# Kernel optimization log

Measured on AMD Instinct MI355X. Metric: run time of the kernel, lower is better.

Reference implementation:

```python
import jax, jax.numpy as jnp
import numpy as np
import math
from jax import lax

N = 5          # kernel_size (hard-coded PHT assumes 5x5)
K = N // 2     # 2
EPS = 1e-6
THETA = 0.7

def _pht_kernel_np():
    # H_i = cos(2*pi*2*r^2 + 0*theta) on the 5x5 grid, times calibrated spectral weights, plus eps
    coords = np.arange(N, dtype=np.float32) - K
    gv, gu = np.meshgrid(coords, coords, indexing='ij')  # torch.meshgrid default is 'ij'
    r2 = (gu ** 2 + gv ** 2) / (K * K + EPS)
    H = np.cos(2.0 * math.pi * 2.0 * r2).astype(np.float32)
    target = np.zeros((N, N), np.float32)
    target[K, K] = -4.0
    target[K - 1, K] = 1.0
    target[K + 1, K] = 1.0
    target[K, K - 1] = 1.0
    target[K, K + 1] = 1.0
    sw = np.where(target != 0, target / H, 0.0).astype(np.float32)
    return (H * sw + EPS).astype(np.float32)  # (5,5)

def _rotation_maps_np():
    # Replicates rotate_kernel exactly: float32 cos/sin, int() truncation, later (h,w) overwrite.
    angles = np.linspace(0, 2 * np.pi, 8, endpoint=False)
    SH = np.zeros((8, N, N), np.int32)
    SW = np.zeros((8, N, N), np.int32)
    M = np.zeros((8, N, N), np.float32)
    for ai, a in enumerate(angles):
        c = float(np.cos(np.float32(a)))
        s = float(np.sin(np.float32(a)))
        for h in range(N):
            for w in range(N):
                rh = int(h * c + w * (-s))
                rw = int(h * s + w * c)
                if 0 <= rh < N and 0 <= rw < N:
                    SH[ai, rh, rw] = h
                    SW[ai, rh, rw] = w
                    M[ai, rh, rw] = 1.0
    return SH, SW, M

_PHT = jnp.asarray(_pht_kernel_np())                     # (5,5)
_sh, _sw, _m = _rotation_maps_np()
_SH = jnp.asarray(_sh)
_SW = jnp.asarray(_sw)
_MASK = jnp.asarray(_m)

def setup_inputs() -> dict:
    key = jax.random.key(0)
    k1, k2 = jax.random.split(key)
    x = jax.random.normal(k1, (32, 64, 128, 128), dtype=jnp.float32)
    weight = jax.random.normal(k2, (64, 64, 5, 5), dtype=jnp.float32) * 0.05
    alpha = jnp.ones((1,), dtype=jnp.float32)
    return {"x": x, "weight": weight, "alpha": alpha}

def reference(x, weight, alpha):
    # Branch 1: PHT-modulated weight, averaged over 8 SO(2) rotations.
    # pht_kernel is (C_in,1,5,5) with identical values per channel -> broadcast (5,5).
    w_eff = weight * alpha[0] * _PHT[None, None]          # (Co,Ci,5,5)
    # rotated[o,i,a,rh,rw] = w_eff[o,i,SH[a,rh,rw],SW[a,rh,rw]] * MASK
    rotated = w_eff[:, :, _SH, _SW] * _MASK               # (Co,Ci,8,5,5)
    # conv is linear in weight: mean of 8 convs == conv with mean kernel
    mean_k = rotated.mean(axis=2)                         # (Co,Ci,5,5)
    out = lax.conv_general_dilated(
        x, mean_k, window_strides=(1, 1), padding=[(2, 2), (2, 2)],
        dimension_numbers=("NCHW", "OIHW", "NCHW"))
    # Branch 2: 1x1 kernel_diff; rotation of a 1x1 kernel is identity, mean of 8 == single conv.
    kd = weight.sum(axis=(2, 3))                          # (Co,Ci)
    out_diff = jnp.einsum("oi,bihw->bohw", kd, x)
    return out - THETA * out_diff
```

## Files before the change

kernel.cpp:

```cpp
#include <hip/hip_runtime.h>
#include <stdint.h>

typedef __attribute__((ext_vector_type(8))) __bf16 bf16x8;
typedef __attribute__((ext_vector_type(16))) float f32x16;
typedef __attribute__((ext_vector_type(4))) unsigned int u32x4;
typedef __attribute__((ext_vector_type(2))) float f32x2;
typedef unsigned int u32;
typedef unsigned short u16;

#define THETA 0.7f

__host__ __device__ constexpr float pht_val(int q) {
  return (q == 12) ? (-4.0f + 1e-6f)
       : (q == 7 || q == 11 || q == 13 || q == 17) ? (1.0f + 1e-6f)
       : 1e-6f;
}

__device__ __forceinline__ u16 f2bf(float v) {
  u32 u = __builtin_bit_cast(u32, v);
  return (u16)((u + 0x7fffu + ((u >> 16) & 1u)) >> 16);
}

__global__ __launch_bounds__(256) void k_prep(const float* __restrict__ wgt,
                                              const float* __restrict__ alpha,
                                              u16* __restrict__ apack) {
  int t = blockIdx.x * 256 + threadIdx.x;
  int o = t >> 6, ci = t & 63;
  const float* wp = wgt + ((size_t)(o * 64 + ci)) * 25;
  float wv[25], sumw = 0.f;
#pragma unroll
  for (int p = 0; p < 25; ++p) { wv[p] = wp[p]; sumw += wv[p]; }
  float keff[25];
#pragma unroll
  for (int p = 0; p < 25; ++p) keff[p] = pht_val(p) * wv[p];
  constexpr int TP[33] = {0,1,2,3,4,6,7,9,12,13,  0,1,2,3,4,  0, 0, 0,
                          0,5,10,15,20,  0,5,6,10,11,12,15,17,20,21};
  constexpr int TQ[33] = {5,6,12,17,23,10,16,22,20,21,  0,5,10,15,20,  5, 0, 5,
                          0,6,7,8,9,  5,6,2,12,8,4,17,9,23,14};
#pragma unroll
  for (int e = 0; e < 33; ++e) keff[TP[e]] += pht_val(TQ[e]) * wv[TQ[e]];

  float al = alpha[0];
  int kc = ci >> 4, oh = o >> 5;
  int lane = ((ci >> 3) & 1) * 32 + (o & 31);
#pragma unroll
  for (int p = 0; p < 25; ++p) {
    float v = al * (keff[p] * 0.125f);
    if (p == 12) v -= THETA * sumw;
    size_t idx = ((((size_t)p * 4 + kc) * 2 + oh) * 64 + lane) * 8 + (ci & 7);
    apack[idx] = f2bf(v);
  }
}

#define ROWB 9216

#define MM(A, B, C) __builtin_amdgcn_mfma_f32_32x32x16_bf16((A), __builtin_bit_cast(bf16x8, (B)), (C), 0, 0, 0)

#define LDBR(S, DX, KC) do {                                                \
    const char* pb_ = pcol + (DX) * 128;                                    \
    int gx_ = ((((KC) * 2 + lhi) ^ ((l31 + (DX)) & 7)) << 4);               \
    br##S##0 = *(const u32x4*)(pb_ + 0 * ROWB + gx_);                       \
    br##S##1 = *(const u32x4*)(pb_ + 1 * ROWB + gx_);                       \
    br##S##2 = *(const u32x4*)(pb_ + 2 * ROWB + gx_);                       \
    br##S##3 = *(const u32x4*)(pb_ + 3 * ROWB + gx_);                       \
    br##S##4 = *(const u32x4*)(pb_ + 4 * ROWB + gx_);                       \
    br##S##5 = *(const u32x4*)(pb_ + 5 * ROWB + gx_);                       \
    br##S##6 = *(const u32x4*)(pb_ + 6 * ROWB + gx_);                       \
    br##S##7 = *(const u32x4*)(pb_ + 7 * ROWB + gx_);                       \
  } while (0)

#define LDAF(S, DX, KC) do {                                                \
    af##S##0 = apb[(size_t)((0 * 5 + (DX)) * 512 + (KC) * 128)];            \
    af##S##1 = apb[(size_t)((1 * 5 + (DX)) * 512 + (KC) * 128)];            \
    af##S##2 = apb[(size_t)((2 * 5 + (DX)) * 512 + (KC) * 128)];            \
    af##S##3 = apb[(size_t)((3 * 5 + (DX)) * 512 + (KC) * 128)];            \
    af##S##4 = apb[(size_t)((4 * 5 + (DX)) * 512 + (KC) * 128)];            \
  } while (0)

#define BURST(S) do {                                                       \
    bf16x8 A_;                                                              \
    A_ = __builtin_bit_cast(bf16x8, af##S##0);                              \
    a0 = MM(A_, br##S##0, a0); a1 = MM(A_, br##S##1, a1);                   \
    a2 = MM(A_, br##S##2, a2); a3 = MM(A_, br##S##3, a3);                   \
    A_ = __builtin_bit_cast(bf16x8, af##S##1);                              \
    a0 = MM(A_, br##S##1, a0); a1 = MM(A_, br##S##2, a1);                   \
    a2 = MM(A_, br##S##3, a2); a3 = MM(A_, br##S##4, a3);                   \
    A_ = __builtin_bit_cast(bf16x8, af##S##2);                              \
    a0 = MM(A_, br##S##2, a0); a1 = MM(A_, br##S##3, a1);                   \
    a2 = MM(A_, br##S##4, a2); a3 = MM(A_, br##S##5, a3);                   \
    A_ = __builtin_bit_cast(bf16x8, af##S##3);                              \
    a0 = MM(A_, br##S##3, a0); a1 = MM(A_, br##S##4, a1);                   \
    a2 = MM(A_, br##S##5, a2); a3 = MM(A_, br##S##6, a3);                   \
    A_ = __builtin_bit_cast(bf16x8, af##S##4);                              \
    a0 = MM(A_, br##S##4, a0); a1 = MM(A_, br##S##5, a1);                   \
    a2 = MM(A_, br##S##6, a2); a3 = MM(A_, br##S##7, a3);                   \
  } while (0)

#define SGB __builtin_amdgcn_sched_group_barrier
#define SCHED_FULL() do {                                                   \
    SGB(0x020, 5, 0);                           \
    SGB(0x100, 2, 0); SGB(0x008, 5, 0);                                     \
    SGB(0x100, 2, 0); SGB(0x008, 5, 0);                                     \
    SGB(0x100, 2, 0); SGB(0x008, 5, 0);                                     \
    SGB(0x100, 2, 0); SGB(0x008, 5, 0);                                     \
  } while (0)

#define ITER(CUR, NXT, DXN, KCN) do {                                       \
    LDBR(NXT, DXN, KCN); LDAF(NXT, DXN, KCN); BURST(CUR); SCHED_FULL();     \
  } while (0)

#define TWR(RB, C, I2, W)                                                   \
  *(u32*)((RB) + (C) * 128 + ((((I2) >> 2) ^ ((C) & 7)) << 4)               \
          + (((I2) & 3) << 2)) = (W)

__global__ __launch_bounds__(256, 2) void k_conv(const float* __restrict__ x,
                                                 const u32x4* __restrict__ apv,
                                                 float* __restrict__ out) {
  __shared__ char tile[8 * ROWB];
  int bid = blockIdx.x;
  int lg = (bid & 7) * 256 + (bid >> 3);
  int ph = lg & 1, yt = (lg >> 1) & 31, n = lg >> 6;
  int y0 = yt * 4, px0 = ph * 64;
  int tid = threadIdx.x;
  int l = tid & 63;

  {
    const float* xn = x + (size_t)n * 64 * 16384;
    int p = tid & 31;
    int i2g = tid >> 5;
    bool hthr = (tid < 128) && !(tid & 2);
    int hi2 = tid >> 2, hp = tid & 1;
    int hpx = hp ? px0 + 64 : px0 - 2;
    int hc = hp ? 66 : 0;
    bool hvalid = (unsigned)hpx < 128u;
#pragma unroll
    for (int rr = 0; rr < 8; ++rr) {
      int sy = y0 + rr - 2;
      bool rowok = (unsigned)sy < 128u;
      char* rowbase = tile + rr * ROWB;
      const float* xr = xn + (size_t)sy * 128;
#pragma unroll
      for (int m = 0; m < 4; ++m) {
        int i2 = i2g * 4 + m;
        f32x2 va = {0.f, 0.f}, vb = {0.f, 0.f};
        if (rowok) {
          const float* pa = xr + (size_t)(2 * i2) * 16384 + px0 + 2 * p;
          va = *(const f32x2*)pa;
          vb = *(const f32x2*)(pa + 16384);
        }
        u32 w0 = (u32)f2bf(va.x) | ((u32)f2bf(vb.x) << 16);
        u32 w1 = (u32)f2bf(va.y) | ((u32)f2bf(vb.y) << 16);
        int c0 = 2 * p + 2;
        TWR(rowbase, c0, i2, w0);
        TWR(rowbase, c0 + 1, i2, w1);
      }
      if (hthr) {
        f32x2 va = {0.f, 0.f}, vb = {0.f, 0.f};
        if (rowok && hvalid) {
          const float* pa = xr + (size_t)(2 * hi2) * 16384 + hpx;
          va = *(const f32x2*)pa;
          vb = *(const f32x2*)(pa + 16384);
        }
        u32 w0 = (u32)f2bf(va.x) | ((u32)f2bf(vb.x) << 16);
        u32 w1 = (u32)f2bf(va.y) | ((u32)f2bf(vb.y) << 16);
        TWR(rowbase, hc, hi2, w0);
        TWR(rowbase, hc + 1, hi2, w1);
      }
    }
  }

  int wv = tid >> 6;
  int oh = wv >> 1, q32 = wv & 1;
  int l31 = l & 31, lhi = l >> 5;
  const u32x4* apb = apv + (size_t)(oh * 64 + l);
  const char* pcol = tile + (q32 * 32 + l31) * 128;

  u32x4 brA0, brA1, brA2, brA3, brA4, brA5, brA6, brA7;
  u32x4 brB0, brB1, brB2, brB3, brB4, brB5, brB6, brB7;
  u32x4 afA0, afA1, afA2, afA3, afA4;
  u32x4 afB0, afB1, afB2, afB3, afB4;

  LDAF(A, 0, 0);
  __syncthreads();
  LDBR(A, 0, 0);

  f32x16 a0 = 0, a1 = 0, a2 = 0, a3 = 0;

  ITER(A, B, 0, 1);
  ITER(B, A, 0, 2);
  ITER(A, B, 0, 3);
  ITER(B, A, 1, 0);
  ITER(A, B, 1, 1);
  ITER(B, A, 1, 2);
  ITER(A, B, 1, 3);
  ITER(B, A, 2, 0);
  ITER(A, B, 2, 1);
  ITER(B, A, 2, 2);
  ITER(A, B, 2, 3);
  ITER(B, A, 3, 0);
  ITER(A, B, 3, 1);
  ITER(B, A, 3, 2);
  ITER(A, B, 3, 3);
  ITER(B, A, 4, 0);
  ITER(A, B, 4, 1);
  ITER(B, A, 4, 2);
  ITER(A, B, 4, 3);
  BURST(B);

  float* ob = out + ((size_t)(n * 64 + oh * 32) * 128 + y0) * 128
              + px0 + q32 * 32 + l31;
#pragma unroll
  for (int rg = 0; rg < 16; ++rg) {
    int orow = (rg & 3) + 8 * (rg >> 2) + 4 * lhi;
    float* obr = ob + (size_t)orow * 16384;
    obr[0]   = a0[rg];
    obr[128] = a1[rg];
    obr[256] = a2[rg];
    obr[384] = a3[rg];
  }
}

extern "C" void kernel_launch(void* const* d_in, const int* in_sizes, int n_in,
                              void* d_out, int out_size, void* d_ws, size_t ws_size,
                              hipStream_t stream) {
  const float* x     = (const float*)d_in[0];
  const float* wgt   = (const float*)d_in[1];
  const float* alpha = (const float*)d_in[2];
  float* out = (float*)d_out;

  u16* apack = (u16*)d_ws;

  k_prep<<<16,   256, 0, stream>>>(wgt, alpha, apack);
  k_conv<<<2048, 256, 0, stream>>>(x, (const u32x4*)apack, out);
}
```

Before: 126.7 us.

## Halve conv tile width to 32 pixels with 128-thread blocks and wider staging

Each block now covers 32 output pixels instead of 64 and runs 2 waves instead of 4, doubling the grid to 4096 blocks and halving the LDS tile. Input staging is rewritten so each thread loads 8 channels at a pixel pair and writes one 16-byte vector per column, with halo columns handled by the first 16 threads. The aim is more resident blocks and better latency hiding from the smaller LDS footprint, plus fewer, wider LDS stores. The cost is a larger halo fraction, which means more redundant global reads of x per output pixel.

New measurement: 131.4 us. +3.7%, slower.

```diff
diff --git a/kernel.cpp b/kernel.cpp
--- a/kernel.cpp
+++ b/kernel.cpp
@@ -52,7 +52,7 @@
   }
 }
 
-#define ROWB 9216
+#define ROWB 4608
 
 #define MM(A, B, C) __builtin_amdgcn_mfma_f32_32x32x16_bf16((A), __builtin_bit_cast(bf16x8, (B)), (C), 0, 0, 0)
 
@@ -109,71 +109,66 @@
     LDBR(NXT, DXN, KCN); LDAF(NXT, DXN, KCN); BURST(CUR); SCHED_FULL();     \
   } while (0)
 
-#define TWR(RB, C, I2, W)                                                   \
-  *(u32*)((RB) + (C) * 128 + ((((I2) >> 2) ^ ((C) & 7)) << 4)               \
-          + (((I2) & 3) << 2)) = (W)
-
-__global__ __launch_bounds__(256, 2) void k_conv(const float* __restrict__ x,
+#define STAGE_SLOT(CP, GG) do {                                             \
+    int pxb_ = px0 + 2 * (CP) - 2;                                          \
+    bool ok_ = rowok && ((unsigned)pxb_ < 128u);                            \
+    const float* ps_ = xr + (size_t)(8 * (GG)) * 16384 + pxb_;              \
+    f32x2 v0 = {0.f, 0.f}, v1 = {0.f, 0.f}, v2 = {0.f, 0.f}, v3 = {0.f, 0.f}; \
+    f32x2 v4 = {0.f, 0.f}, v5 = {0.f, 0.f}, v6 = {0.f, 0.f}, v7 = {0.f, 0.f}; \
+    if (ok_) {                                                              \
+      v0 = *(const f32x2*)(ps_);                                            \
+      v1 = *(const f32x2*)(ps_ + 16384);                                    \
+      v2 = *(const f32x2*)(ps_ + 2 * 16384);                                \
+      v3 = *(const f32x2*)(ps_ + 3 * 16384);                                \
+      v4 = *(const f32x2*)(ps_ + 4 * 16384);                                \
+      v5 = *(const f32x2*)(ps_ + 5 * 16384);                                \
+      v6 = *(const f32x2*)(ps_ + 6 * 16384);                                \
+      v7 = *(const f32x2*)(ps_ + 7 * 16384);                                \
+    }                                                                       \
+    u32x4 wx_, wy_;                                                         \
+    wx_[0] = (u32)f2bf(v0.x) | ((u32)f2bf(v1.x) << 16);                     \
+    wx_[1] = (u32)f2bf(v2.x) | ((u32)f2bf(v3.x) << 16);                     \
+    wx_[2] = (u32)f2bf(v4.x) | ((u32)f2bf(v5.x) << 16);                     \
+    wx_[3] = (u32)f2bf(v6.x) | ((u32)f2bf(v7.x) << 16);                     \
+    wy_[0] = (u32)f2bf(v0.y) | ((u32)f2bf(v1.y) << 16);                     \
+    wy_[1] = (u32)f2bf(v2.y) | ((u32)f2bf(v3.y) << 16);                     \
+    wy_[2] = (u32)f2bf(v4.y) | ((u32)f2bf(v5.y) << 16);                     \
+    wy_[3] = (u32)f2bf(v6.y) | ((u32)f2bf(v7.y) << 16);                     \
+    int c0_ = 2 * (CP);                                                     \
+    *(u32x4*)(rowbase + c0_ * 128 + (((GG) ^ (c0_ & 7)) << 4)) = wx_;       \
+    *(u32x4*)(rowbase + (c0_ + 1) * 128 + (((GG) ^ ((c0_ + 1) & 7)) << 4)) = wy_; \
+  } while (0)
+
+__global__ __launch_bounds__(128, 2) void k_conv(const float* __restrict__ x,
                                                  const u32x4* __restrict__ apv,
                                                  float* __restrict__ out) {
   __shared__ char tile[8 * ROWB];
   int bid = blockIdx.x;
-  int lg = (bid & 7) * 256 + (bid >> 3);
-  int ph = lg & 1, yt = (lg >> 1) & 31, n = lg >> 6;
-  int y0 = yt * 4, px0 = ph * 64;
+  int lg = (bid & 7) * 512 + (bid >> 3);
+  int pxq = lg & 3, yt = (lg >> 2) & 31, n = lg >> 7;
+  int y0 = yt * 4, px0 = pxq * 32;
   int tid = threadIdx.x;
   int l = tid & 63;
 
   {
-    const float* xn = x + (size_t)n * 64 * 16384;
-    int p = tid & 31;
-    int i2g = tid >> 5;
-    bool hthr = (tid < 128) && !(tid & 2);
-    int hi2 = tid >> 2, hp = tid & 1;
-    int hpx = hp ? px0 + 64 : px0 - 2;
-    int hc = hp ? 66 : 0;
-    bool hvalid = (unsigned)hpx < 128u;
+    const float* xn = x + (size_t)n * (64 * 16384);
+    int sp = tid & 15, sg = tid >> 4;
+    int hp = 16 + (tid >> 3), hg = tid & 7;
 #pragma unroll
     for (int rr = 0; rr < 8; ++rr) {
       int sy = y0 + rr - 2;
       bool rowok = (unsigned)sy < 128u;
       char* rowbase = tile + rr * ROWB;
       const float* xr = xn + (size_t)sy * 128;
-#pragma unroll
-      for (int m = 0; m < 4; ++m) {
-        int i2 = i2g * 4 + m;
-        f32x2 va = {0.f, 0.f}, vb = {0.f, 0.f};
-        if (rowok) {
-          const float* pa = xr + (size_t)(2 * i2) * 16384 + px0 + 2 * p;
-          va = *(const f32x2*)pa;
-          vb = *(const f32x2*)(pa + 16384);
-        }
-        u32 w0 = (u32)f2bf(va.x) | ((u32)f2bf(vb.x) << 16);
-        u32 w1 = (u32)f2bf(va.y) | ((u32)f2bf(vb.y) << 16);
-        int c0 = 2 * p + 2;
-        TWR(rowbase, c0, i2, w0);
-        TWR(rowbase, c0 + 1, i2, w1);
-      }
-      if (hthr) {
-        f32x2 va = {0.f, 0.f}, vb = {0.f, 0.f};
-        if (rowok && hvalid) {
-          const float* pa = xr + (size_t)(2 * hi2) * 16384 + hpx;
-          va = *(const f32x2*)pa;
-          vb = *(const f32x2*)(pa + 16384);
-        }
-        u32 w0 = (u32)f2bf(va.x) | ((u32)f2bf(vb.x) << 16);
-        u32 w1 = (u32)f2bf(va.y) | ((u32)f2bf(vb.y) << 16);
-        TWR(rowbase, hc, hi2, w0);
-        TWR(rowbase, hc + 1, hi2, w1);
-      }
+      STAGE_SLOT(sp, sg);
+      if (tid < 16) STAGE_SLOT(hp, hg);
     }
   }
 
-  int wv = tid >> 6;
-  int oh = wv >> 1, q32 = wv & 1;
+  int oh = tid >> 6;
   int l31 = l & 31, lhi = l >> 5;
   const u32x4* apb = apv + (size_t)(oh * 64 + l);
-  const char* pcol = tile + (q32 * 32 + l31) * 128;
+  const char* pcol = tile + l31 * 128;
 
   u32x4 brA0, brA1, brA2, brA3, brA4, brA5, brA6, brA7;
   u32x4 brB0, brB1, brB2, brB3, brB4, brB5, brB6, brB7;
@@ -208,7 +203,7 @@
   BURST(B);
 
   float* ob = out + ((size_t)(n * 64 + oh * 32) * 128 + y0) * 128
-              + px0 + q32 * 32 + l31;
+              + px0 + l31;
 #pragma unroll
   for (int rg = 0; rg < 16; ++rg) {
     int orow = (rg & 3) + 8 * (rg >> 2) + 4 * lhi;
@@ -231,5 +226,5 @@
   u16* apack = (u16*)d_ws;
 
   k_prep<<<16,   256, 0, stream>>>(wgt, alpha, apack);
-  k_conv<<<2048, 256, 0, stream>>>(x, (const u32x4*)apack, out);
-}
+  k_conv<<<4096, 128, 0, stream>>>(x, (const u32x4*)apack, out);
+}
```

## Pipeline input tile staging per channel chunk with MFMA compute

Applied to the files above, without the earlier changes.

Restructures the conv kernel so the input tile is loaded and converted to bf16 in four channel chunks, with the global loads and LDS writes of the next chunk interleaved between the MFMA iterations of the current chunk. The loop order changes to run channel chunk outermost and kernel column innermost, with a barrier after each phase. Loads become wider float4 accesses per thread and use the hardware packed bf16 convert instruction, and the tile column layout is shifted by two for alignment. The aim is to hide the global-load and convert prologue behind compute, at the cost of more barriers, more register pressure and a more complex schedule.

New measurement: 116.2 us. -8.3%, faster.

```diff
diff --git a/kernel.cpp b/kernel.cpp
--- a/kernel.cpp
+++ b/kernel.cpp
@@ -4,6 +4,7 @@
 typedef __attribute__((ext_vector_type(8))) __bf16 bf16x8;
 typedef __attribute__((ext_vector_type(16))) float f32x16;
 typedef __attribute__((ext_vector_type(4))) unsigned int u32x4;
+typedef __attribute__((ext_vector_type(4))) float f32x4;
 typedef __attribute__((ext_vector_type(2))) float f32x2;
 typedef unsigned int u32;
 typedef unsigned short u16;
@@ -56,9 +57,13 @@
 
 #define MM(A, B, C) __builtin_amdgcn_mfma_f32_32x32x16_bf16((A), __builtin_bit_cast(bf16x8, (B)), (C), 0, 0, 0)
 
+#define PK2(A_, B_) ({ u32 r_;                                              \
+    asm("v_cvt_pk_bf16_f32 %0, %1, %2" : "=v"(r_) : "v"(A_), "v"(B_));      \
+    r_; })
+
 #define LDBR(S, DX, KC) do {                                                \
     const char* pb_ = pcol + (DX) * 128;                                    \
-    int gx_ = ((((KC) * 2 + lhi) ^ ((l31 + (DX)) & 7)) << 4);               \
+    int gx_ = ((((KC) * 2 + lhi) ^ ((l31 + (DX) + 2) & 7)) << 4);           \
     br##S##0 = *(const u32x4*)(pb_ + 0 * ROWB + gx_);                       \
     br##S##1 = *(const u32x4*)(pb_ + 1 * ROWB + gx_);                       \
     br##S##2 = *(const u32x4*)(pb_ + 2 * ROWB + gx_);                       \
@@ -98,7 +103,7 @@
 
 #define SGB __builtin_amdgcn_sched_group_barrier
 #define SCHED_FULL() do {                                                   \
-    SGB(0x020, 5, 0);                           \
+    SGB(0x020, 5, 0);                                                       \
     SGB(0x100, 2, 0); SGB(0x008, 5, 0);                                     \
     SGB(0x100, 2, 0); SGB(0x008, 5, 0);                                     \
     SGB(0x100, 2, 0); SGB(0x008, 5, 0);                                     \
@@ -109,9 +114,75 @@
     LDBR(NXT, DXN, KCN); LDAF(NXT, DXN, KCN); BURST(CUR); SCHED_FULL();     \
   } while (0)
 
-#define TWR(RB, C, I2, W)                                                   \
-  *(u32*)((RB) + (C) * 128 + ((((I2) >> 2) ^ ((C) & 7)) << 4)               \
-          + (((I2) & 3) << 2)) = (W)
+#define TBAR() do {                                                         \
+    asm volatile("s_waitcnt lgkmcnt(0)" ::: "memory");                      \
+    __builtin_amdgcn_sched_barrier(0);                                      \
+    __builtin_amdgcn_s_barrier();                                           \
+    __builtin_amdgcn_sched_barrier(0);                                      \
+  } while (0)
+
+#define SLOADP(P) do {                                                      \
+    if (rowok) {                                                            \
+      const float* pm_ = xrow + (size_t)(16 * (P) + 8 * gp) * 16384 + pxm;  \
+      sm0 = *(const f32x4*)(pm_);              sm1 = *(const f32x4*)(pm_ + 16384);      \
+      sm2 = *(const f32x4*)(pm_ + 2 * 16384);  sm3 = *(const f32x4*)(pm_ + 3 * 16384);  \
+      sm4 = *(const f32x4*)(pm_ + 4 * 16384);  sm5 = *(const f32x4*)(pm_ + 5 * 16384);  \
+      sm6 = *(const f32x4*)(pm_ + 6 * 16384);  sm7 = *(const f32x4*)(pm_ + 7 * 16384);  \
+    } else {                                                                \
+      sm0 = 0; sm1 = 0; sm2 = 0; sm3 = 0; sm4 = 0; sm5 = 0; sm6 = 0; sm7 = 0; \
+    }                                                                       \
+    if (hdut) {                                                             \
+      if (hok) {                                                            \
+        const float* ph_ = xn + (size_t)hsy * 128                           \
+                           + (size_t)(16 * (P) + 8 * hgp) * 16384 + hpx;    \
+        sh0 = *(const f32x2*)(ph_);              sh1 = *(const f32x2*)(ph_ + 16384);     \
+        sh2 = *(const f32x2*)(ph_ + 2 * 16384);  sh3 = *(const f32x2*)(ph_ + 3 * 16384); \
+        sh4 = *(const f32x2*)(ph_ + 4 * 16384);  sh5 = *(const f32x2*)(ph_ + 5 * 16384); \
+        sh6 = *(const f32x2*)(ph_ + 6 * 16384);  sh7 = *(const f32x2*)(ph_ + 7 * 16384); \
+      } else {                                                              \
+        sh0 = 0; sh1 = 0; sh2 = 0; sh3 = 0; sh4 = 0; sh5 = 0; sh6 = 0; sh7 = 0; \
+      }                                                                     \
+    }                                                                       \
+  } while (0)
+
+#define SWRITEP(P) do {                                                     \
+    int g_ = 2 * (P) + gp;                                                  \
+    u32x4 w_;                                                               \
+    w_[0] = PK2(sm0.x, sm1.x); w_[1] = PK2(sm2.x, sm3.x);                   \
+    w_[2] = PK2(sm4.x, sm5.x); w_[3] = PK2(sm6.x, sm7.x);                   \
+    *(u32x4*)(rowbase + cbm * 128 + ((g_ ^ (cbm & 7)) << 4)) = w_;          \
+    w_[0] = PK2(sm0.y, sm1.y); w_[1] = PK2(sm2.y, sm3.y);                   \
+    w_[2] = PK2(sm4.y, sm5.y); w_[3] = PK2(sm6.y, sm7.y);                   \
+    *(u32x4*)(rowbase + (cbm + 1) * 128 + ((g_ ^ ((cbm + 1) & 7)) << 4)) = w_; \
+    w_[0] = PK2(sm0.z, sm1.z); w_[1] = PK2(sm2.z, sm3.z);                   \
+    w_[2] = PK2(sm4.z, sm5.z); w_[3] = PK2(sm6.z, sm7.z);                   \
+    *(u32x4*)(rowbase + (cbm + 2) * 128 + ((g_ ^ ((cbm + 2) & 7)) << 4)) = w_; \
+    w_[0] = PK2(sm0.w, sm1.w); w_[1] = PK2(sm2.w, sm3.w);                   \
+    w_[2] = PK2(sm4.w, sm5.w); w_[3] = PK2(sm6.w, sm7.w);                   \
+    *(u32x4*)(rowbase + (cbm + 3) * 128 + ((g_ ^ ((cbm + 3) & 7)) << 4)) = w_; \
+    if (hdut) {                                                             \
+      int hg_ = 2 * (P) + hgp;                                              \
+      u32x4 u_;                                                             \
+      u_[0] = PK2(sh0.x, sh1.x); u_[1] = PK2(sh2.x, sh3.x);                 \
+      u_[2] = PK2(sh4.x, sh5.x); u_[3] = PK2(sh6.x, sh7.x);                 \
+      *(u32x4*)(hrowbase + hc * 128 + ((hg_ ^ (hc & 7)) << 4)) = u_;        \
+      u_[0] = PK2(sh0.y, sh1.y); u_[1] = PK2(sh2.y, sh3.y);                 \
+      u_[2] = PK2(sh4.y, sh5.y); u_[3] = PK2(sh6.y, sh7.y);                 \
+      *(u32x4*)(hrowbase + (hc + 1) * 128 + ((hg_ ^ ((hc + 1) & 7)) << 4)) = u_; \
+    }                                                                       \
+  } while (0)
+
+#define CPHASE(SP, CP) do {                                                 \
+    SLOADP(SP);                                                             \
+    LDBR(A, 0, CP); LDAF(A, 0, CP);                                         \
+    ITER(A, B, 1, CP);                                                      \
+    ITER(B, A, 2, CP);                                                      \
+    SWRITEP(SP);                                                            \
+    ITER(A, B, 3, CP);                                                      \
+    ITER(B, A, 4, CP);                                                      \
+    BURST(A);                                                               \
+    TBAR();                                                                 \
+  } while (0)
 
 __global__ __launch_bounds__(256, 2) void k_conv(const float* __restrict__ x,
                                                  const u32x4* __restrict__ apv,
@@ -124,88 +195,49 @@
   int tid = threadIdx.x;
   int l = tid & 63;
 
-  {
-    const float* xn = x + (size_t)n * 64 * 16384;
-    int p = tid & 31;
-    int i2g = tid >> 5;
-    bool hthr = (tid < 128) && !(tid & 2);
-    int hi2 = tid >> 2, hp = tid & 1;
-    int hpx = hp ? px0 + 64 : px0 - 2;
-    int hc = hp ? 66 : 0;
-    bool hvalid = (unsigned)hpx < 128u;
-#pragma unroll
-    for (int rr = 0; rr < 8; ++rr) {
-      int sy = y0 + rr - 2;
-      bool rowok = (unsigned)sy < 128u;
-      char* rowbase = tile + rr * ROWB;
-      const float* xr = xn + (size_t)sy * 128;
-#pragma unroll
-      for (int m = 0; m < 4; ++m) {
-        int i2 = i2g * 4 + m;
-        f32x2 va = {0.f, 0.f}, vb = {0.f, 0.f};
-        if (rowok) {
-          const float* pa = xr + (size_t)(2 * i2) * 16384 + px0 + 2 * p;
-          va = *(const f32x2*)pa;
-          vb = *(const f32x2*)(pa + 16384);
-        }
-        u32 w0 = (u32)f2bf(va.x) | ((u32)f2bf(vb.x) << 16);
-        u32 w1 = (u32)f2bf(va.y) | ((u32)f2bf(vb.y) << 16);
-        int c0 = 2 * p + 2;
-        TWR(rowbase, c0, i2, w0);
-        TWR(rowbase, c0 + 1, i2, w1);
-      }
-      if (hthr) {
-        f32x2 va = {0.f, 0.f}, vb = {0.f, 0.f};
-        if (rowok && hvalid) {
-          const float* pa = xr + (size_t)(2 * hi2) * 16384 + hpx;
-          va = *(const f32x2*)pa;
-          vb = *(const f32x2*)(pa + 16384);
-        }
-        u32 w0 = (u32)f2bf(va.x) | ((u32)f2bf(vb.x) << 16);
-        u32 w1 = (u32)f2bf(va.y) | ((u32)f2bf(vb.y) << 16);
-        TWR(rowbase, hc, hi2, w0);
-        TWR(rowbase, hc + 1, hi2, w1);
-      }
-    }
-  }
+  const float* xn = x + (size_t)n * (64 * 16384);
+  int rr = tid >> 5, qq = (tid >> 1) & 15, gp = tid & 1;
+  int sy = y0 + rr - 2;
+  bool rowok = (unsigned)sy < 128u;
+  const float* xrow = xn + (size_t)(rowok ? sy : 0) * 128;
+  int pxm = px0 + 4 * qq;
+  int cbm = 4 + 4 * qq;
+  char* rowbase = tile + rr * ROWB;
+  bool hdut = tid < 32;
+  int hrr = tid >> 2, hside = (tid >> 1) & 1, hgp = tid & 1;
+  int hpx = hside ? px0 + 64 : px0 - 2;
+  int hc = hside ? 68 : 2;
+  int hsy = y0 + hrr - 2;
+  bool hok = ((unsigned)hpx < 127u) && ((unsigned)hsy < 128u);
+  if (!hok) hsy = 0; if (hpx < 0) hpx = 0;
+  char* hrowbase = tile + hrr * ROWB;
 
   int wv = tid >> 6;
   int oh = wv >> 1, q32 = wv & 1;
   int l31 = l & 31, lhi = l >> 5;
   const u32x4* apb = apv + (size_t)(oh * 64 + l);
-  const char* pcol = tile + (q32 * 32 + l31) * 128;
-
+  const char* pcol = tile + (q32 * 32 + l31 + 2) * 128;
+
+  f32x4 sm0, sm1, sm2, sm3, sm4, sm5, sm6, sm7;
+  f32x2 sh0, sh1, sh2, sh3, sh4, sh5, sh6, sh7;
   u32x4 brA0, brA1, brA2, brA3, brA4, brA5, brA6, brA7;
   u32x4 brB0, brB1, brB2, brB3, brB4, brB5, brB6, brB7;
   u32x4 afA0, afA1, afA2, afA3, afA4;
   u32x4 afB0, afB1, afB2, afB3, afB4;
-
-  LDAF(A, 0, 0);
-  __syncthreads();
-  LDBR(A, 0, 0);
-
   f32x16 a0 = 0, a1 = 0, a2 = 0, a3 = 0;
 
-  ITER(A, B, 0, 1);
-  ITER(B, A, 0, 2);
-  ITER(A, B, 0, 3);
-  ITER(B, A, 1, 0);
-  ITER(A, B, 1, 1);
-  ITER(B, A, 1, 2);
+  SLOADP(0);
+  SWRITEP(0);
+  TBAR();
+  CPHASE(1, 0);
+  CPHASE(2, 1);
+  CPHASE(3, 2);
+  LDBR(A, 0, 3); LDAF(A, 0, 3);
   ITER(A, B, 1, 3);
-  ITER(B, A, 2, 0);
-  ITER(A, B, 2, 1);
-  ITER(B, A, 2, 2);
-  ITER(A, B, 2, 3);
-  ITER(B, A, 3, 0);
-  ITER(A, B, 3, 1);
-  ITER(B, A, 3, 2);
+  ITER(B, A, 2, 3);
   ITER(A, B, 3, 3);
-  ITER(B, A, 4, 0);
-  ITER(A, B, 4, 1);
-  ITER(B, A, 4, 2);
-  ITER(A, B, 4, 3);
-  BURST(B);
+  ITER(B, A, 4, 3);
+  BURST(A);
 
   float* ob = out + ((size_t)(n * 64 + oh * 32) * 128 + y0) * 128
               + px0 + q32 * 32 + l31;
```
